# Performance work log

Measured on AMD Instinct MI355X. Metric: run time of the kernel, lower is better.

## Reference

```python
import jax, jax.numpy as jnp
import numpy as np

D = 512      # hidden_size
H = 8        # num_heads
DK = D // H  # head dim
B, T = 8, 1024
EPS = 1e-5


def setup_inputs() -> dict:
    key = jax.random.key(0)
    ks = jax.random.split(key, 12)
    s = 0.02
    return {
        "x": jax.random.normal(ks[0], (B, T, D), jnp.float32),
        "xlens": jax.random.randint(ks[1], (B,), 1, T + 1, jnp.int32),
        "pos_emb": jax.random.normal(ks[2], (1, 2 * T - 1, D), jnp.float32),
        "ln_gamma": jnp.ones((D,), jnp.float32),
        "ln_beta": jnp.zeros((D,), jnp.float32),
        "Wq": jax.random.normal(ks[3], (D, D), jnp.float32) * s,
        "bq": jnp.zeros((D,), jnp.float32),
        "Wk": jax.random.normal(ks[4], (D, D), jnp.float32) * s,
        "bk": jnp.zeros((D,), jnp.float32),
        "Wv": jax.random.normal(ks[5], (D, D), jnp.float32) * s,
        "bv": jnp.zeros((D,), jnp.float32),
        "Wpos": jax.random.normal(ks[6], (D, D), jnp.float32) * s,  # no bias
        "pos_bias_u": jax.random.normal(ks[7], (H, DK), jnp.float32) * s,
        "pos_bias_v": jax.random.normal(ks[8], (H, DK), jnp.float32) * s,
        "Wo": jax.random.normal(ks[9], (D, D), jnp.float32) * s,
        "bo": jnp.zeros((D,), jnp.float32),
    }


def _rel_shift(x):
    # Transformer-XL shift trick: (B, H, T, 2T-1) -> (B, H, T, T)
    b, h, t, n = x.shape
    x = jnp.pad(x, ((0, 0), (0, 0), (0, 0), (1, 0)))       # (b,h,t,2t)
    x = x.reshape(b, h, n + 1, t)[:, :, 1:, :].reshape(b, h, t, n)
    return x[..., :t]


def reference(x, xlens, pos_emb, ln_gamma, ln_beta, Wq, bq, Wk, bk, Wv, bv,
              Wpos, pos_bias_u, pos_bias_v, Wo, bo):
    b, t, d = x.shape
    # LayerNorm
    mu = jnp.mean(x, axis=-1, keepdims=True)
    var = jnp.mean(jnp.square(x - mu), axis=-1, keepdims=True)
    xn = (x - mu) * jax.lax.rsqrt(var + EPS) * ln_gamma + ln_beta

    # key padding mask: True where index >= len (padded)
    pad_mask = jnp.arange(t)[None, :] >= xlens[:, None]      # (B, T)

    q = (xn @ Wq + bq).reshape(b, t, H, DK)                  # (B,T,H,DK)
    k = (xn @ Wk + bk).reshape(b, t, H, DK)
    v = (xn @ Wv + bv).reshape(b, t, H, DK)
    p = (pos_emb @ Wpos).reshape(-1, H, DK)                  # (2T-1,H,DK)

    q_u = q + pos_bias_u                                     # (B,T,H,DK)
    q_v = q + pos_bias_v

    # content score + positional score (Transformer-XL)
    matrix_ac = jnp.einsum('bthd,bshd->bhts', q_u, k)        # (B,H,T,T)
    matrix_bd = jnp.einsum('bthd,nhd->bhtn', q_v, p)         # (B,H,T,2T-1)
    matrix_bd = _rel_shift(matrix_bd)                        # (B,H,T,T)

    scores = (matrix_ac + matrix_bd) / jnp.sqrt(jnp.float32(DK))
    scores = jnp.where(pad_mask[:, None, None, :], jnp.float32(-1e9), scores)
    attn = jax.nn.softmax(scores, axis=-1)
    attn = jnp.where(pad_mask[:, None, None, :], 0.0, attn)
    # dropout prob applied only in training; eval mode -> identity

    out = jnp.einsum('bhts,bshd->bthd', attn, v).reshape(b, t, d)
    out = out @ Wo + bo
    return out, xlens
```

## Files before the change

### kernel.cpp

```cpp
#include <hip/hip_runtime.h>
#include <stdint.h>


typedef __attribute__((ext_vector_type(8))) short s8v;
typedef __attribute__((ext_vector_type(4))) short s4v;
typedef __attribute__((ext_vector_type(4))) float f4v;
typedef unsigned short u16;

#define MFMA(a, b, c) __builtin_amdgcn_mfma_f32_16x16x32_bf16((a), (b), (c), 0, 0, 0)

__device__ __forceinline__ float bf2f(u16 u) {
    union { unsigned i; float f; } w; w.i = ((unsigned)u) << 16; return w.f;
}
__device__ __forceinline__ u16 f2bf(float f) {
    union { float f; unsigned i; } w; w.f = f;
    return (u16)((w.i + 0x7FFFu + ((w.i >> 16) & 1u)) >> 16);
}
__device__ __forceinline__ u16 f2bt(float f) {
    union { float f; unsigned i; } w; w.f = f;
    return (u16)(w.i >> 16);
}
__device__ __forceinline__ void gld16(const void* g, void* l) {
    __builtin_amdgcn_global_load_lds(
        (const __attribute__((address_space(1))) unsigned int*)g,
        (__attribute__((address_space(3))) unsigned int*)l, 16, 0, 0);
}

__global__ __launch_bounds__(256) void prep_k(
    const float* __restrict__ Wq, const float* __restrict__ Wk, const float* __restrict__ Wv,
    const float* __restrict__ Wpos, const float* __restrict__ Wo,
    const float* __restrict__ pos_emb, const int* __restrict__ xlens,
    const float* __restrict__ x, const float* __restrict__ gamma,
    const float* __restrict__ beta,
    u16* __restrict__ wt, u16* __restrict__ pe, float* __restrict__ tail,
    u16* __restrict__ xn)
{
    int bid = blockIdx.x, tid = threadIdx.x;
    if (bid < 1280) {
        __shared__ float lt[32][33];
        int mat = bid >> 8, tile = bid & 255;
        int kt = (tile >> 4) << 5, nt = (tile & 15) << 5;
        const float* W = mat == 0 ? Wq : mat == 1 ? Wk : mat == 2 ? Wv : mat == 3 ? Wpos : Wo;
        int ty = tid >> 3, tx = tid & 7;
        float4 vv = *(const float4*)&W[(kt + ty) * 512 + nt + tx * 4];
        lt[ty][tx * 4 + 0] = vv.x; lt[ty][tx * 4 + 1] = vv.y;
        lt[ty][tx * 4 + 2] = vv.z; lt[ty][tx * 4 + 3] = vv.w;
        __syncthreads();
        int nl = tid >> 3, k4 = (tid & 7) * 4;
        union { s4v v; u16 u[4]; } ob;
        #pragma unroll
        for (int e = 0; e < 4; ++e) ob.u[e] = f2bf(lt[k4 + e][nl]);
        *(s4v*)&wt[mat * 262144 + (nt + nl) * 512 + kt + k4] = ob.v;
    } else if (bid < 2304) {
        int i = (bid - 1280) * 1024 + tid * 4;
        union { s4v v; u16 u[4]; } ob;
        if (i < 2047 * 512) {
            float4 vv = *(const float4*)&pos_emb[i];
            ob.u[0] = f2bf(vv.x); ob.u[1] = f2bf(vv.y);
            ob.u[2] = f2bf(vv.z); ob.u[3] = f2bf(vv.w);
        } else {
            ob.u[0] = ob.u[1] = ob.u[2] = ob.u[3] = 0;
        }
        *(s4v*)&pe[i] = ob.v;
    } else if (bid == 2304) {
        if (tid < 8) tail[tid] = (float)xlens[tid];
    } else {
        int tok = (bid - 2305) * 4 + (tid >> 6);
        int l = tid & 63;
        const float* xr = x + (size_t)tok * 512 + l * 8;
        float v[8];
        {
            float4 a = *(const float4*)xr; float4 b = *(const float4*)(xr + 4);
            v[0] = a.x; v[1] = a.y; v[2] = a.z; v[3] = a.w;
            v[4] = b.x; v[5] = b.y; v[6] = b.z; v[7] = b.w;
        }
        float s = 0.f, q = 0.f;
        #pragma unroll
        for (int e = 0; e < 8; ++e) { s += v[e]; q += v[e] * v[e]; }
        #pragma unroll
        for (int off = 1; off < 64; off <<= 1) { s += __shfl_xor(s, off); q += __shfl_xor(q, off); }
        float mean = s * (1.f / 512.f);
        float var = q * (1.f / 512.f) - mean * mean;
        float inv = rsqrtf(var + 1e-5f);
        union { s8v v; u16 u[8]; } ob;
        #pragma unroll
        for (int e = 0; e < 8; ++e)
            ob.u[e] = f2bf((v[e] - mean) * inv * gamma[l * 8 + e] + beta[l * 8 + e]);
        *(s8v*)&xn[(size_t)tok * 512 + l * 8] = ob.v;
    }
}

__global__ __launch_bounds__(256, 2) void gemm_k(
    const u16* __restrict__ A, const u16* __restrict__ Ap, const u16* __restrict__ wt,
    const float* __restrict__ bq, const float* __restrict__ bk, const float* __restrict__ bv,
    int mode, u16* __restrict__ qo, u16* __restrict__ ko, u16* __restrict__ vtg,
    u16* __restrict__ pb, float* __restrict__ of)
{
    __shared__ u16 Al[2][128 * 64];
    __shared__ u16 Bl[2][128 * 64];
    int tid = threadIdx.x, l = tid & 63, wid = tid >> 6;
    int wr = wid >> 1, wc = wid & 1, r = l & 15, g = l >> 4;
    int m0, nb, mat;
    const u16 *Ag, *Wg;
    if (mode == 0) {
        if (blockIdx.y < 12) {
            m0 = blockIdx.x << 7; int n0 = blockIdx.y << 7;
            mat = n0 >> 9; nb = n0 & 511; Ag = A; Wg = wt + mat * 262144;
        } else {
            mat = 3; m0 = (blockIdx.x & 15) << 7; nb = (blockIdx.x >> 4) << 7;
            Ag = Ap; Wg = wt + 3 * 262144;
        }
    } else {
        mat = 4; m0 = blockIdx.x << 7; nb = blockIdx.y << 7; Ag = A; Wg = wt + 4 * 262144;
    }

    int rw8 = l >> 3;
    int csw = ((l & 7) ^ rw8) << 3;
    int off0 = ((g ^ (r & 7)) << 3);
    int off1 = (((4 + g) ^ (r & 7)) << 3);

    f4v zero = {0.f, 0.f, 0.f, 0.f};
    f4v acc[4][4];
    #pragma unroll
    for (int i = 0; i < 4; ++i)
        #pragma unroll
        for (int j = 0; j < 4; ++j) acc[i][j] = zero;

    #pragma unroll
    for (int it = 0; it < 4; ++it) {
        int rowb = wid * 32 + it * 8;
        gld16(&Ag[(size_t)(m0 + rowb + rw8) * 512 + csw], &Al[0][rowb * 64]);
        gld16(&Wg[(size_t)(nb + rowb + rw8) * 512 + csw], &Bl[0][rowb * 64]);
    }
    __syncthreads();

    for (int t = 0; t < 8; ++t) {
        int cur = t & 1;
        if (t < 7) {
            int k1 = (t + 1) << 6;
            #pragma unroll
            for (int it = 0; it < 4; ++it) {
                int rowb = wid * 32 + it * 8;
                gld16(&Ag[(size_t)(m0 + rowb + rw8) * 512 + k1 + csw], &Al[cur ^ 1][rowb * 64]);
                gld16(&Wg[(size_t)(nb + rowb + rw8) * 512 + k1 + csw], &Bl[cur ^ 1][rowb * 64]);
            }
        }
        s8v af[4][2], bfv[4][2];
        #pragma unroll
        for (int i = 0; i < 4; ++i) {
            int row = (wr * 64 + i * 16 + r) * 64;
            af[i][0] = *(const s8v*)&Al[cur][row + off0];
            af[i][1] = *(const s8v*)&Al[cur][row + off1];
        }
        #pragma unroll
        for (int j = 0; j < 4; ++j) {
            int row = (wc * 64 + j * 16 + r) * 64;
            bfv[j][0] = *(const s8v*)&Bl[cur][row + off0];
            bfv[j][1] = *(const s8v*)&Bl[cur][row + off1];
        }
        __builtin_amdgcn_s_setprio(1);
        #pragma unroll
        for (int i = 0; i < 4; ++i)
            #pragma unroll
            for (int j = 0; j < 4; ++j) {
                acc[i][j] = MFMA(af[i][0], bfv[j][0], acc[i][j]);
                acc[i][j] = MFMA(af[i][1], bfv[j][1], acc[i][j]);
            }
        __builtin_amdgcn_s_setprio(0);
        __syncthreads();
    }

    #pragma unroll
    for (int i = 0; i < 4; ++i)
        #pragma unroll
        for (int j = 0; j < 4; ++j) {
            int ncol = nb + wc * 64 + j * 16 + r;
            int mbase = m0 + wr * 64 + i * 16 + g * 4;
            if (mode == 2) {
                float bb = bq[ncol];
                #pragma unroll
                for (int jj = 0; jj < 4; ++jj)
                    of[(size_t)(mbase + jj) * 512 + ncol] = acc[i][j][jj] + bb;
            } else if (mat == 3) {
                int hh = ncol >> 6, dk = ncol & 63;
                #pragma unroll
                for (int jj = 0; jj < 4; ++jj) {
                    int m = mbase + jj;
                    if (m < 2047) pb[(hh * 2047 + m) * 64 + dk] = f2bf(acc[i][j][jj]);
                }
            } else if (mat == 2) {
                float bb = bv[ncol];
                int hh = ncol >> 6, dk = ncol & 63;
                int bbx = mbase >> 10, t = mbase & 1023;
                union { s4v v; u16 u[4]; } pk;
                #pragma unroll
                for (int jj = 0; jj < 4; ++jj) pk.u[jj] = f2bf(acc[i][j][jj] + bb);
                *(s4v*)&vtg[((size_t)(bbx * 8 + hh) * 64 + dk) * 1024 + t] = pk.v;
            } else {
                float bb = (mat == 0 ? bq : bk)[ncol];
                u16* dst = (mat == 0) ? qo : ko;
                int hh = ncol >> 6, dk = ncol & 63;
                #pragma unroll
                for (int jj = 0; jj < 4; ++jj) {
                    int m = mbase + jj;
                    int bbx = m >> 10, t = m & 1023;
                    dst[((size_t)(bbx * 8 + hh) * 1024 + t) * 64 + dk] = f2bf(acc[i][j][jj] + bb);
                }
            }
        }
}

__global__ __launch_bounds__(512, 4) void attn_k(
    const u16* __restrict__ q, const u16* __restrict__ k, const u16* __restrict__ vtg,
    const u16* __restrict__ p, const float* __restrict__ pbu, const float* __restrict__ pbv,
    const int* __restrict__ xlens, u16* __restrict__ ao)
{
    __shared__ u16 Ks[2][64 * 64];
    __shared__ u16 Vt[64 * 64];
    __shared__ u16 Ps[256 * 64];
    __shared__ u16 Tb[8][16 * 72];

    int tid = threadIdx.x, l = tid & 63, wid = tid >> 6;
    int r = l & 15, g = l >> 4, kq = g << 3;
    int t0 = blockIdx.x << 7;
    int bh = blockIdx.y, b = bh & 7, h = bh >> 3;
    int tw = t0 + wid * 16;
    int xlen = xlens[b];
    const u16* qh = q + (size_t)(b * 8 + h) * 65536;
    const u16* kh = k + (size_t)(b * 8 + h) * 65536;
    const u16* vh = vtg + (size_t)(b * 8 + h) * 65536;
    const u16* ph = p + (size_t)h * 2047 * 64;

    int rw8 = l >> 3;
    int csw = ((l & 7) ^ rw8) << 3;
    int off0 = ((g ^ (r & 7)) << 3);
    int off1 = (((4 + g) ^ (r & 7)) << 3);

    const float SCALE = 0.18033688f;

    s8v qu[2], qv[2];
    #pragma unroll
    for (int ks = 0; ks < 2; ++ks) {
        union { s8v v; u16 u[8]; } src, du, dv;
        src.v = *(const s8v*)&qh[(tw + r) * 64 + ks * 32 + kq];
        float4 u0 = *(const float4*)&pbu[h * 64 + ks * 32 + kq];
        float4 u1 = *(const float4*)&pbu[h * 64 + ks * 32 + kq + 4];
        float4 v0 = *(const float4*)&pbv[h * 64 + ks * 32 + kq];
        float4 v1 = *(const float4*)&pbv[h * 64 + ks * 32 + kq + 4];
        float ub[8] = {u0.x, u0.y, u0.z, u0.w, u1.x, u1.y, u1.z, u1.w};
        float vb_[8] = {v0.x, v0.y, v0.z, v0.w, v1.x, v1.y, v1.z, v1.w};
        #pragma unroll
        for (int e = 0; e < 8; ++e) {
            float qf = bf2f(src.u[e]);
            du.u[e] = f2bf((qf + ub[e]) * SCALE);
            dv.u[e] = f2bf((qf + vb_[e]) * SCALE);
        }
        qu[ks] = du.v; qv[ks] = dv.v;
    }

    int B0 = 896 - t0;
    int nst = (xlen + 63) >> 6;

    {
        int rowb = wid * 8;
        gld16(&kh[(rowb + rw8) * 64 + csw], &Ks[0][rowb * 64]);
        gld16(&vh[(rowb + rw8) * 1024 + csw], &Vt[rowb * 64]);
    }
    #pragma unroll
    for (int it = 0; it < 3; ++it) {
        int row = wid * 24 + it * 8;
        int slot = (B0 + row) & 255;
        gld16(&ph[(size_t)(B0 + row + rw8) * 64 + csw], &Ps[slot * 64]);
    }
    __syncthreads();

    float lst[4] = {0.f, 0.f, 0.f, 0.f};
    f4v zero = {0.f, 0.f, 0.f, 0.f};
    f4v o[4] = {zero, zero, zero, zero};
    u16* tb = &Tb[wid][0];

    for (int i = 0; i < nst; ++i) {
        int cur = i & 1, s0 = i << 6;
        if (i > 0) {
            int rowb = wid * 8;
            gld16(&vh[(rowb + rw8) * 1024 + s0 + csw], &Vt[rowb * 64]);
        }
        if (i + 1 < nst) {
            int s1 = s0 + 64;
            int rowb = wid * 8;
            gld16(&kh[(s1 + rowb + rw8) * 64 + csw], &Ks[cur ^ 1][rowb * 64]);
            int chunk = B0 + 192 + s0 + wid * 8;
            int slot = chunk & 255;
            int gp = chunk + rw8; gp = gp > 2046 ? 2046 : gp;
            gld16(&ph[(size_t)gp * 64 + csw], &Ps[slot * 64]);
        }
        const u16* KB = &Ks[cur][0];
        f4v st4[4];
        __builtin_amdgcn_s_setprio(1);
        #pragma unroll
        for (int nf = 0; nf < 4; ++nf) {
            int row = (nf * 16 + r) * 64;
            s8v k0 = *(const s8v*)&KB[row + off0];
            s8v k1 = *(const s8v*)&KB[row + off1];
            st4[nf] = MFMA(qu[1], k1, MFMA(qu[0], k0, zero));
        }
        int pstart = 1008 + s0 - tw;
        f4v bst[5];
        #pragma unroll
        for (int pf = 0; pf < 5; ++pf) {
            int slot = (pstart + pf * 16 + r) & 255;
            const u16* rowp = &Ps[slot * 64];
            f4v a = MFMA(qv[0], *(const s8v*)&rowp[off0], zero);
            bst[pf] = MFMA(qv[1], *(const s8v*)&rowp[off1], a);
        }
        __builtin_amdgcn_s_setprio(0);
        bool full = (s0 + 64 <= xlen);
        float pr[4][4];
        #pragma unroll
        for (int j = 0; j < 4; ++j) {
            int tl = g * 4 + j;
            int d = r + 15 - tl;
            int al = ((g << 4) | (d & 15)) << 2;
            unsigned w0 = (unsigned)f2bt(bst[0][j]) | ((unsigned)f2bt(bst[1][j]) << 16);
            unsigned w1 = (unsigned)f2bt(bst[2][j]) | ((unsigned)f2bt(bst[3][j]) << 16);
            unsigned w2 = (unsigned)f2bt(bst[4][j]);
            unsigned p0 = (unsigned)__builtin_amdgcn_ds_bpermute(al, (int)w0);
            unsigned p1 = (unsigned)__builtin_amdgcn_ds_bpermute(al, (int)w1);
            unsigned p2 = (unsigned)__builtin_amdgcn_ds_bpermute(al, (int)w2);
            bool lo = d < 16;
            float bds[4];
            bds[0] = bf2f((u16)(lo ? (p0 & 0xffffu) : (p0 >> 16)));
            bds[1] = bf2f((u16)(lo ? (p0 >> 16) : (p1 & 0xffffu)));
            bds[2] = bf2f((u16)(lo ? (p1 & 0xffffu) : (p1 >> 16)));
            bds[3] = bf2f((u16)(lo ? (p1 >> 16) : (p2 & 0xffffu)));
            #pragma unroll
            for (int nf = 0; nf < 4; ++nf) {
                float e = exp2f(st4[nf][j] + bds[nf]);
                if (!full) e = (s0 + nf * 16 + r >= xlen) ? 0.f : e;
                pr[nf][j] = e;
            }
        }
        #pragma unroll
        for (int j = 0; j < 4; ++j)
            lst[j] += (pr[0][j] + pr[1][j]) + (pr[2][j] + pr[3][j]);
        #pragma unroll
        for (int nf = 0; nf < 4; ++nf)
            #pragma unroll
            for (int j = 0; j < 4; ++j)
                tb[(g * 4 + j) * 72 + nf * 16 + r] = f2bt(pr[nf][j]);
        asm volatile("s_waitcnt lgkmcnt(0)" ::: "memory");
        __builtin_amdgcn_sched_barrier(0);
        s8v pa0 = *(const s8v*)&tb[r * 72 + kq];
        s8v pa1 = *(const s8v*)&tb[r * 72 + 32 + kq];
        if (i > 0) {
            if (i + 1 < nst) asm volatile("s_waitcnt vmcnt(2)" ::: "memory");
            else             asm volatile("s_waitcnt vmcnt(0)" ::: "memory");
        }
        __builtin_amdgcn_s_setprio(1);
        #pragma unroll
        for (int i2 = 0; i2 < 4; ++i2) {
            int vrow = (i2 * 16 + r) * 64;
            o[i2] = MFMA(pa0, *(const s8v*)&Vt[vrow + off0], o[i2]);
            o[i2] = MFMA(pa1, *(const s8v*)&Vt[vrow + off1], o[i2]);
        }
        __builtin_amdgcn_s_setprio(0);
        __syncthreads();
    }
    #pragma unroll
    for (int j = 0; j < 4; ++j) {
        float rs = lst[j];
        rs += __shfl_xor(rs, 1); rs += __shfl_xor(rs, 2);
        rs += __shfl_xor(rs, 4); rs += __shfl_xor(rs, 8);
        float inv = 1.f / rs;
        int t = tw + g * 4 + j;
        #pragma unroll
        for (int i2 = 0; i2 < 4; ++i2)
            ao[((size_t)(b * 1024 + t)) * 512 + h * 64 + i2 * 16 + r] = f2bf(o[i2][j] * inv);
    }
}

extern "C" void kernel_launch(void* const* d_in, const int* in_sizes, int n_in,
                              void* d_out, int out_size, void* d_ws, size_t ws_size,
                              hipStream_t stream)
{
    (void)in_sizes; (void)n_in; (void)out_size; (void)ws_size;
    const float* x     = (const float*)d_in[0];
    const int*   xlens = (const int*)d_in[1];
    const float* pos_e = (const float*)d_in[2];
    const float* gam   = (const float*)d_in[3];
    const float* bet   = (const float*)d_in[4];
    const float* Wq    = (const float*)d_in[5];
    const float* bq    = (const float*)d_in[6];
    const float* Wk    = (const float*)d_in[7];
    const float* bk    = (const float*)d_in[8];
    const float* Wv    = (const float*)d_in[9];
    const float* bv    = (const float*)d_in[10];
    const float* Wpos  = (const float*)d_in[11];
    const float* pbu   = (const float*)d_in[12];
    const float* pbv   = (const float*)d_in[13];
    const float* Wo    = (const float*)d_in[14];
    const float* bo    = (const float*)d_in[15];
    float* out = (float*)d_out;

    char* ws = (char*)d_ws;
    u16* xn  = (u16*)(ws);
    u16* qb  = (u16*)(ws + 8388608);
    u16* kb  = (u16*)(ws + 16777216);
    u16* vtg = (u16*)(ws + 25165824);
    u16* pbf = (u16*)(ws + 33554432);
    u16* pe  = (u16*)(ws + 35651584);
    u16* wt  = (u16*)(ws + 37748736);

    prep_k<<<4353, 256, 0, stream>>>(Wq, Wk, Wv, Wpos, Wo, pos_e, xlens,
                                     x, gam, bet, wt, pe,
                                     out + (size_t)8192 * 512, xn);
    gemm_k<<<dim3(64, 13), 256, 0, stream>>>(xn, pe, wt, bq, bk, bv, 0,
                                             qb, kb, vtg, pbf, nullptr);
    attn_k<<<dim3(8, 64), 512, 0, stream>>>(qb, kb, vtg, pbf, pbu, pbv, xlens, xn);
    gemm_k<<<dim3(64, 4), 256, 0, stream>>>(xn, nullptr, wt, bo, nullptr, nullptr, 2,
                                            nullptr, nullptr, nullptr, nullptr, out);
}
```

Measured before the change: 102.1 us.

## Deepen GEMM pipeline to 4-stage K=32 ring with counted vmcnt waits

The projection GEMM now uses four LDS buffers of K=32 slices instead of two of K=64. Three slices are prefetched ahead, and each step waits with an explicit vmcnt count plus one barrier, replacing the full __syncthreads per iteration. The swizzle is rewritten for 32-wide rows. The aim is to hide global-load latency and cut barrier stalls, at the cost of twice as many loop iterations and fewer MFMAs between barriers.

```diff
diff --git a/kernel.cpp b/kernel.cpp
--- a/kernel.cpp
+++ b/kernel.cpp
@@ -96,8 +96,8 @@
     int mode, u16* __restrict__ qo, u16* __restrict__ ko, u16* __restrict__ vtg,
     u16* __restrict__ pb, float* __restrict__ of)
 {
-    __shared__ u16 Al[2][128 * 64];
-    __shared__ u16 Bl[2][128 * 64];
+    __shared__ u16 Al[4][128 * 32];
+    __shared__ u16 Bl[4][128 * 32];
     int tid = threadIdx.x, l = tid & 63, wid = tid >> 6;
     int wr = wid >> 1, wc = wid & 1, r = l & 15, g = l >> 4;
     int m0, nb, mat;
@@ -114,10 +114,9 @@
         mat = 4; m0 = blockIdx.x << 7; nb = blockIdx.y << 7; Ag = A; Wg = wt + 4 * 262144;
     }
 
-    int rw8 = l >> 3;
-    int csw = ((l & 7) ^ rw8) << 3;
-    int off0 = ((g ^ (r & 7)) << 3);
-    int off1 = (((4 + g) ^ (r & 7)) << 3);
+    int sr4 = l >> 2;
+    int csw2 = (((l & 3) ^ ((l >> 2) & 3) ^ (l >> 4)) << 3);
+    int offK = ((g ^ ((r & 3) ^ (r >> 2))) << 3);
 
     f4v zero = {0.f, 0.f, 0.f, 0.f};
     f4v acc[4][4];
@@ -127,47 +126,45 @@
         for (int j = 0; j < 4; ++j) acc[i][j] = zero;
 
     #pragma unroll
-    for (int it = 0; it < 4; ++it) {
-        int rowb = wid * 32 + it * 8;
-        gld16(&Ag[(size_t)(m0 + rowb + rw8) * 512 + csw], &Al[0][rowb * 64]);
-        gld16(&Wg[(size_t)(nb + rowb + rw8) * 512 + csw], &Bl[0][rowb * 64]);
-    }
-    __syncthreads();
-
-    for (int t = 0; t < 8; ++t) {
-        int cur = t & 1;
-        if (t < 7) {
-            int k1 = (t + 1) << 6;
-            #pragma unroll
-            for (int it = 0; it < 4; ++it) {
-                int rowb = wid * 32 + it * 8;
-                gld16(&Ag[(size_t)(m0 + rowb + rw8) * 512 + k1 + csw], &Al[cur ^ 1][rowb * 64]);
-                gld16(&Wg[(size_t)(nb + rowb + rw8) * 512 + k1 + csw], &Bl[cur ^ 1][rowb * 64]);
-            }
-        }
-        s8v af[4][2], bfv[4][2];
-        #pragma unroll
-        for (int i = 0; i < 4; ++i) {
-            int row = (wr * 64 + i * 16 + r) * 64;
-            af[i][0] = *(const s8v*)&Al[cur][row + off0];
-            af[i][1] = *(const s8v*)&Al[cur][row + off1];
-        }
-        #pragma unroll
-        for (int j = 0; j < 4; ++j) {
-            int row = (wc * 64 + j * 16 + r) * 64;
-            bfv[j][0] = *(const s8v*)&Bl[cur][row + off0];
-            bfv[j][1] = *(const s8v*)&Bl[cur][row + off1];
-        }
+    for (int t = 0; t < 3; ++t) {
+        #pragma unroll
+        for (int it = 0; it < 2; ++it) {
+            int rowb = wid * 32 + it * 16;
+            gld16(&Ag[(size_t)(m0 + rowb + sr4) * 512 + t * 32 + csw2], &Al[t][rowb * 32]);
+            gld16(&Wg[(size_t)(nb + rowb + sr4) * 512 + t * 32 + csw2], &Bl[t][rowb * 32]);
+        }
+    }
+
+    for (int t = 0; t < 16; ++t) {
+        int buf = t & 3;
+        if (t < 14)       asm volatile("s_waitcnt vmcnt(8)" ::: "memory");
+        else if (t == 14) asm volatile("s_waitcnt vmcnt(4)" ::: "memory");
+        else              asm volatile("s_waitcnt vmcnt(0)" ::: "memory");
+        __builtin_amdgcn_s_barrier();
+        asm volatile("" ::: "memory");
+        s8v af[4], bfv[4];
+        #pragma unroll
+        for (int i = 0; i < 4; ++i)
+            af[i] = *(const s8v*)&Al[buf][(wr * 64 + i * 16 + r) * 32 + offK];
+        #pragma unroll
+        for (int j = 0; j < 4; ++j)
+            bfv[j] = *(const s8v*)&Bl[buf][(wc * 64 + j * 16 + r) * 32 + offK];
         __builtin_amdgcn_s_setprio(1);
         #pragma unroll
         for (int i = 0; i < 4; ++i)
             #pragma unroll
-            for (int j = 0; j < 4; ++j) {
-                acc[i][j] = MFMA(af[i][0], bfv[j][0], acc[i][j]);
-                acc[i][j] = MFMA(af[i][1], bfv[j][1], acc[i][j]);
+            for (int j = 0; j < 4; ++j)
+                acc[i][j] = MFMA(af[i], bfv[j], acc[i][j]);
+        __builtin_amdgcn_s_setprio(0);
+        if (t + 3 < 16) {
+            int k1 = (t + 3) << 5, nbuf = (t + 3) & 3;
+            #pragma unroll
+            for (int it = 0; it < 2; ++it) {
+                int rowb = wid * 32 + it * 16;
+                gld16(&Ag[(size_t)(m0 + rowb + sr4) * 512 + k1 + csw2], &Al[nbuf][rowb * 32]);
+                gld16(&Wg[(size_t)(nb + rowb + sr4) * 512 + k1 + csw2], &Bl[nbuf][rowb * 32]);
             }
-        __builtin_amdgcn_s_setprio(0);
-        __syncthreads();
+        }
     }
 
     #pragma unroll
```

New measurement: 108.5 us. 1.06x slower.
